# Kernel tuning notes

Hardware: AMD Instinct MI355X
Metric: run time of the kernel (lower is better)

## Reference

```python
import jax, jax.numpy as jnp
import numpy as np


def conv1d(x, w, b, pad):
    # x: [B, C, L], w: [O, C, K], torch nn.Conv1d semantics (cross-correlation + bias)
    y = jax.lax.conv_general_dilated(
        x, w, window_strides=(1,), padding=[(pad, pad)],
        dimension_numbers=("NCH", "OIH", "NCH"))
    return y + b[None, :, None]


def setup_inputs() -> dict:
    key = jax.random.key(0)
    ks = jax.random.split(key, 11)
    B, C, L = 32, 4, 65536
    def rn(k, shape, fan_in):
        # kaiming-ish scale so activations stay sane
        return jax.random.normal(k, shape, dtype=jnp.float32) / np.sqrt(fan_in)
    return {
        "x": jax.random.normal(ks[0], (B, C, L), dtype=jnp.float32),
        "w_motif": rn(ks[1], (40, 4, 51), 4 * 51),
        "b_motif": jnp.zeros((40,), jnp.float32),
        "w_reduce": rn(ks[2], (4, 40, 1), 40),
        "b_reduce": jnp.zeros((4,), jnp.float32),
        "w_fft": rn(ks[3], (4, 4, 401), 4 * 401),
        "b_fft": jnp.zeros((4,), jnp.float32),
        "w_expand": rn(ks[4], (40, 4, 1), 4),
        "b_expand": jnp.zeros((40,), jnp.float32),
        "w_effect": rn(ks[5], (2, 40, 601), 40 * 601),
        "b_effect": jnp.zeros((2,), jnp.float32),
    }


def reference(x, w_motif, b_motif, w_reduce, b_reduce, w_fft, b_fft,
              w_expand, b_expand, w_effect, b_effect):
    # motif layer + softplus
    y = jax.nn.softplus(conv1d(x, w_motif, b_motif, 25))          # [B,40,L]
    # synergy: factorized FFT-conv block (reduce 1x1 -> long conv -> expand 1x1)
    s = conv1d(y, w_reduce, b_reduce, 0)                          # [B,4,L]
    s = conv1d(s, w_fft, b_fft, 200)                              # [B,4,L]
    s = conv1d(s, w_expand, b_expand, 0)                          # [B,40,L]
    motifact = jax.nn.sigmoid(s) * y                              # gated
    # effect: long conv -> sigmoid
    y_pred = jax.nn.sigmoid(conv1d(motifact, w_effect, b_effect, 300))  # [B,2,L]
    return y_pred[:, :, 500:-500]
```

## Files before the change

### kernel.cpp

```cpp
#include <hip/hip_runtime.h>
#include <hip/hip_bf16.h>
#include <math.h>

#define LEN 65536
#define LOUT 64536
typedef __hip_bfloat16 bf16;
typedef __attribute__((ext_vector_type(8))) short short8;
typedef __attribute__((ext_vector_type(4))) float f32x4;

__device__ inline float b2f(bf16 h) { return __bfloat162float(h); }
__device__ inline bf16 f2b(float f) { return __float2bfloat16(f); }
__device__ inline float us2f(unsigned short u) { bf16 h = *(bf16*)&u; return __bfloat162float(h); }
__device__ inline float softplus_f(float v) {
    return fmaxf(v, 0.f) + __logf(1.f + __expf(-fabsf(v)));
}

__global__ __launch_bounds__(256) void k_x2b(const float* __restrict__ x,
                                             short* __restrict__ xb, int n8) {
    int i = blockIdx.x * 256 + threadIdx.x;
    if (i >= n8) return;
    const float* src = x + (size_t)i * 8;
    float4 f0 = *(const float4*)src;
    float4 f1 = *(const float4*)(src + 4);
    short8 v; bf16 h;
    h = f2b(f0.x); v[0] = *(short*)&h;
    h = f2b(f0.y); v[1] = *(short*)&h;
    h = f2b(f0.z); v[2] = *(short*)&h;
    h = f2b(f0.w); v[3] = *(short*)&h;
    h = f2b(f1.x); v[4] = *(short*)&h;
    h = f2b(f1.y); v[5] = *(short*)&h;
    h = f2b(f1.z); v[6] = *(short*)&h;
    h = f2b(f1.w); v[7] = *(short*)&h;
    *(short8*)(xb + (size_t)i * 8) = v;
}

__global__ __launch_bounds__(256) void k_prep_mot(const float* __restrict__ w_motif,
                                                  short* __restrict__ fragA) {
    int idx = blockIdx.x * 256 + threadIdx.x;
    if (idx >= 40 * 4 * 3 * 64 * 8) return;
    int i = idx & 7;
    int lane = (idx >> 3) & 63;
    int rest = idx >> 9;
    int qc = rest % 3; rest /= 3;
    int c = rest & 3; int o = rest >> 2;
    int dlt = lane & 15, kb = lane >> 4;
    int m = 32 * qc + 8 * kb + i;
    int k = m - 7 - dlt;
    float v = (k >= 0 && k < 51) ? w_motif[(o * 4 + c) * 51 + k] : 0.f;
    bf16 h = f2b(v);
    fragA[idx] = *(short*)&h;
}

#define MOT_BLKS 522
#define MOT_PAD  528
__global__ __launch_bounds__(256, 2) void k_motif_mfma(const short* __restrict__ xb,
        const short* __restrict__ fragA, const float* __restrict__ b_motif,
        const float* __restrict__ w_reduce, const float* __restrict__ b_reduce,
        bf16* __restrict__ y, bf16* __restrict__ s1, int b0) {
    __shared__ __align__(16) short bwin[4][MOT_PAD * 8];
    const int tid = threadIdx.x;
    const int lane = tid & 63, wv = tid >> 6;
    const int wg = blockIdx.x, bl = blockIdx.y;
    const int bg = b0 + bl;
    const int L0 = wg * 4096;
    const int win0 = L0 - 32;
    const int ln15 = lane & 15, lkb = lane >> 4;

    #pragma unroll 1
    for (int c = 0; c < 4; ++c) {
        const short* src = xb + ((size_t)bg * 4 + c) * LEN;
        for (int Lb = tid; Lb < MOT_BLKS; Lb += 256) {
            int gi = win0 + Lb * 8;
            short8 v;
            if (gi >= 0 && gi + 8 <= LEN) {
                v = *(const short8*)(src + gi);
            } else {
                #pragma unroll
                for (int j = 0; j < 8; ++j)
                    v[j] = (gi + j >= 0 && gi + j < LEN) ? src[gi + j] : (short)0;
            }
            int Pb = Lb ^ ((Lb >> 3) & 7);
            *(short8*)(&bwin[c][Pb * 8]) = v;
        }
    }
    __syncthreads();

    float s1a[4][4][4];
    #pragma unroll
    for (int nt = 0; nt < 4; ++nt)
        #pragma unroll
        for (int c = 0; c < 4; ++c) {
            float bc = b_reduce[c];
            #pragma unroll
            for (int j = 0; j < 4; ++j) s1a[nt][c][j] = bc;
        }

    #pragma unroll 1
    for (int og = 0; og < 10; ++og) {
        f32x4 acc[4][4];
        #pragma unroll
        for (int Mt = 0; Mt < 4; ++Mt)
            #pragma unroll
            for (int nt = 0; nt < 4; ++nt)
                acc[Mt][nt] = (f32x4){0.f, 0.f, 0.f, 0.f};

        #pragma unroll 1
        for (int c = 0; c < 4; ++c) {
            short8 afc[4][3];
            #pragma unroll
            for (int Mt = 0; Mt < 4; ++Mt)
                #pragma unroll
                for (int qc = 0; qc < 3; ++qc)
                    afc[Mt][qc] = *(const short8*)(fragA +
                        (size_t)(((og * 4 + Mt) * 12 + c * 3 + qc) * 64 + lane) * 8);
            #pragma unroll
            for (int nt = 0; nt < 4; ++nt) {
                const int tt = wv * 4 + nt;
                #pragma unroll
                for (int qc = 0; qc < 3; ++qc) {
                    int L = 32 * tt + 2 * ln15 + 4 * qc + lkb;
                    int P = L ^ ((L >> 3) & 7);
                    short8 bfr = *(const short8*)(&bwin[c][P * 8]);
                    #pragma unroll
                    for (int Mt = 0; Mt < 4; ++Mt)
                        acc[Mt][nt] = __builtin_amdgcn_mfma_f32_16x16x32_bf16(
                            afc[Mt][qc], bfr, acc[Mt][nt], 0, 0, 0);
                }
            }
        }

        #pragma unroll
        for (int Mt = 0; Mt < 4; ++Mt) {
            const int o = og * 4 + Mt;
            const float bb = b_motif[o];
            const float wr0 = w_reduce[0 * 40 + o], wr1 = w_reduce[1 * 40 + o];
            const float wr2 = w_reduce[2 * 40 + o], wr3 = w_reduce[3 * 40 + o];
            #pragma unroll
            for (int nt = 0; nt < 4; ++nt) {
                int tt = wv * 4 + nt;
                int pos = L0 + tt * 256 + 16 * ln15 + 4 * lkb;
                float v0 = softplus_f(acc[Mt][nt][0] + bb);
                float v1 = softplus_f(acc[Mt][nt][1] + bb);
                float v2 = softplus_f(acc[Mt][nt][2] + bb);
                float v3 = softplus_f(acc[Mt][nt][3] + bb);
                ushort4 st; bf16 h;
                h = f2b(v0); st.x = *(unsigned short*)&h;
                h = f2b(v1); st.y = *(unsigned short*)&h;
                h = f2b(v2); st.z = *(unsigned short*)&h;
                h = f2b(v3); st.w = *(unsigned short*)&h;
                *(ushort4*)(&y[((size_t)bl * 40 + o) * LEN + pos]) = st;
                s1a[nt][0][0] += wr0 * v0; s1a[nt][0][1] += wr0 * v1;
                s1a[nt][0][2] += wr0 * v2; s1a[nt][0][3] += wr0 * v3;
                s1a[nt][1][0] += wr1 * v0; s1a[nt][1][1] += wr1 * v1;
                s1a[nt][1][2] += wr1 * v2; s1a[nt][1][3] += wr1 * v3;
                s1a[nt][2][0] += wr2 * v0; s1a[nt][2][1] += wr2 * v1;
                s1a[nt][2][2] += wr2 * v2; s1a[nt][2][3] += wr2 * v3;
                s1a[nt][3][0] += wr3 * v0; s1a[nt][3][1] += wr3 * v1;
                s1a[nt][3][2] += wr3 * v2; s1a[nt][3][3] += wr3 * v3;
            }
        }
    }

    #pragma unroll
    for (int nt = 0; nt < 4; ++nt) {
        int tt = wv * 4 + nt;
        int pos = L0 + tt * 256 + 16 * ln15 + 4 * lkb;
        #pragma unroll
        for (int c = 0; c < 4; ++c) {
            ushort4 st; bf16 h;
            h = f2b(s1a[nt][c][0]); st.x = *(unsigned short*)&h;
            h = f2b(s1a[nt][c][1]); st.y = *(unsigned short*)&h;
            h = f2b(s1a[nt][c][2]); st.z = *(unsigned short*)&h;
            h = f2b(s1a[nt][c][3]); st.w = *(unsigned short*)&h;
            *(ushort4*)(&s1[((size_t)bl * 4 + c) * LEN + pos]) = st;
        }
    }
}

__global__ __launch_bounds__(256) void k_prep_fft(const float* __restrict__ w_fft,
                                                  short* __restrict__ fragA) {
    int idx = blockIdx.x * 256 + threadIdx.x;
    if (idx >= 4 * 7 * 4 * 2 * 64 * 8) return;
    int i = idx & 7;
    int lane = (idx >> 3) & 63;
    int rest = idx >> 9;
    int ql = rest & 1; rest >>= 1;
    int Mt = rest & 3; rest >>= 2;
    int qb = rest % 7; int c = rest / 7;
    int dlt = lane & 15, kb = lane >> 4;
    int kkp = 32 * (qb * 2 + ql) + 8 * kb + i;
    int kk = kkp - dlt;
    float v = (kk >= 0 && kk < 401) ? w_fft[(Mt * 4 + c) * 401 + kk] : 0.f;
    bf16 h = f2b(v);
    fragA[idx] = *(short*)&h;
}

#define FFT_BLKS 568
__global__ __launch_bounds__(256) void k_fft(const short* __restrict__ s1,
        const short* __restrict__ fragA, const float* __restrict__ b_fft,
        bf16* __restrict__ s2) {
    __shared__ __align__(16) short bwin[4][FFT_BLKS * 8];
    const int tid = threadIdx.x;
    const int lane = tid & 63, wv = tid >> 6;
    const int wg = blockIdx.x, bl = blockIdx.y;
    const int P0 = wg * 4096;
    const int win0 = P0 - 200;
    const int ln15 = lane & 15, lkb = lane >> 4;

    f32x4 acc[4][4];
    #pragma unroll
    for (int Mt = 0; Mt < 4; ++Mt)
        #pragma unroll
        for (int nt = 0; nt < 4; ++nt)
            acc[Mt][nt] = (f32x4){0.f, 0.f, 0.f, 0.f};

    #pragma unroll 1
    for (int cl = 0; cl < 4; ++cl) {
        const short* src = s1 + ((size_t)bl * 4 + cl) * LEN;
        for (int Lb = tid; Lb < FFT_BLKS; Lb += 256) {
            int gi = win0 + Lb * 8;
            short8 v;
            if (gi >= 0 && gi + 8 <= LEN) {
                v = *(const short8*)(src + gi);
            } else {
                #pragma unroll
                for (int j = 0; j < 8; ++j)
                    v[j] = (gi + j >= 0 && gi + j < LEN) ? src[gi + j] : (short)0;
            }
            int Pb = Lb ^ ((Lb >> 3) & 7);
            *(short8*)(&bwin[cl][Pb * 8]) = v;
        }
    }
    __syncthreads();

    #pragma unroll 1
    for (int cl = 0; cl < 4; ++cl) {
        #pragma unroll 1
        for (int qb = 0; qb < 7; ++qb) {
            short8 af[4][2];
            #pragma unroll
            for (int Mt = 0; Mt < 4; ++Mt)
                #pragma unroll
                for (int ql = 0; ql < 2; ++ql)
                    af[Mt][ql] = *(const short8*)(fragA +
                        (size_t)((((cl * 7 + qb) * 4 + Mt) * 2 + ql) * 64 + lane) * 8);
            #pragma unroll
            for (int nt = 0; nt < 4; ++nt) {
                const int tt = wv * 4 + nt;
                #pragma unroll
                for (int ql = 0; ql < 2; ++ql) {
                    int qc = qb * 2 + ql;
                    int L = 2 * ln15 + lkb + 4 * qc + 32 * tt;
                    int P = L ^ ((L >> 3) & 7);
                    short8 bfr = *(const short8*)(&bwin[cl][P * 8]);
                    #pragma unroll
                    for (int Mt = 0; Mt < 4; ++Mt)
                        acc[Mt][nt] = __builtin_amdgcn_mfma_f32_16x16x32_bf16(
                            af[Mt][ql], bfr, acc[Mt][nt], 0, 0, 0);
                }
            }
        }
    }

    #pragma unroll
    for (int Mt = 0; Mt < 4; ++Mt) {
        float bb = b_fft[Mt];
        #pragma unroll
        for (int nt = 0; nt < 4; ++nt) {
            int tt = wv * 4 + nt;
            int pos = P0 + tt * 256 + 16 * ln15 + 4 * lkb;
            ushort4 st; bf16 h;
            h = f2b(acc[Mt][nt][0] + bb); st.x = *(unsigned short*)&h;
            h = f2b(acc[Mt][nt][1] + bb); st.y = *(unsigned short*)&h;
            h = f2b(acc[Mt][nt][2] + bb); st.z = *(unsigned short*)&h;
            h = f2b(acc[Mt][nt][3] + bb); st.w = *(unsigned short*)&h;
            *(ushort4*)(&s2[((size_t)bl * 4 + Mt) * LEN + pos]) = st;
        }
    }
}

__global__ __launch_bounds__(256) void k_prep(const float* __restrict__ w_eff,
                                              short* __restrict__ fragA) {
    int idx = blockIdx.x * 256 + threadIdx.x;
    if (idx >= 40 * 4 * 2 * 5 * 64 * 8) return;
    int i = idx & 7;
    int lane = (idx >> 3) & 63;
    int rest = idx >> 9;
    int ql = rest % 5; rest /= 5;
    int Mt = rest & 1; rest >>= 1;
    int qb = rest & 3; int c = rest >> 2;
    int q = qb * 5 + ql;
    int dlt = lane & 15, kb = lane >> 4;
    int kp = 32 * q + 8 * kb + i;
    int kk = kp - dlt;
    float v = (kk >= 0 && kk < 601) ? w_eff[(Mt * 40 + c) * 601 + kk] : 0.f;
    bf16 h = __float2bfloat16(v);
    fragA[idx] = *(short*)&h;
}

#define EFF_NBLK 336
#define EFF_SH (EFF_NBLK * 8)
__device__ __forceinline__ void eff_prefetch(const short* __restrict__ mact,
        size_t chanBase, int cc, int tid, int win0, short8 (&yreg)[2][4]) {
    #pragma unroll
    for (int it = 0; it < 2; ++it) {
        int Lb = tid + it * 256;
        if (Lb < EFF_NBLK) {
            int gi = win0 + Lb * 8;
            bool full = (gi + 8 <= LEN);
            #pragma unroll
            for (int ch = 0; ch < 4; ++ch) {
                const short* src = mact + (chanBase + cc * 4 + ch) * (size_t)LEN;
                short8 v = {0, 0, 0, 0, 0, 0, 0, 0};
                if (full) {
                    v = *(const short8*)(src + gi);
                } else {
                    #pragma unroll
                    for (int j = 0; j < 8; ++j)
                        v[j] = (gi + j < LEN) ? src[gi + j] : (short)0;
                }
                yreg[it][ch] = v;
            }
        }
    }
}

__global__ __launch_bounds__(256, 3) void k_effect(const short* __restrict__ mact,
        const short* __restrict__ s2,
        const short* __restrict__ fragA,
        const float* __restrict__ w_expand, const float* __restrict__ b_expand,
        float* __restrict__ part) {
    __shared__ __align__(16) char smem[2 * EFF_SH * 4 * 2 + 160 * 4 + 40 * 4];
    short (*bwin)[EFF_SH]  = (short(*)[EFF_SH])smem;
    short (*s2win)[EFF_SH] = (short(*)[EFF_SH])(smem + EFF_SH * 4 * 2);
    float* wexp = (float*)(smem + 2 * EFF_SH * 4 * 2);
    float* bexp = wexp + 160;
    float* red  = (float*)smem;

    const int tid = threadIdx.x;
    const int lane = tid & 63, wv = tid >> 6;
    const int wgl = blockIdx.x, bl = blockIdx.y, half = blockIdx.z;
    const int coff = half * 20;
    const int L0 = wgl * 2048;
    const int win0 = L0 + 200;
    const int ln15 = lane & 15, lkb = lane >> 4;
    const size_t chanBase = (size_t)bl * 40 + coff;

    if (tid < 160) wexp[tid] = w_expand[tid];
    if (tid < 40) bexp[tid] = b_expand[tid];
    #pragma unroll 1
    for (int c = 0; c < 4; ++c) {
        const short* sp = s2 + ((size_t)bl * 4 + c) * LEN;
        for (int Lb = tid; Lb < EFF_NBLK; Lb += 256) {
            int gi = win0 + Lb * 8;
            short8 v = {0, 0, 0, 0, 0, 0, 0, 0};
            if (gi + 8 <= LEN) {
                v = *(const short8*)(sp + gi);
            } else {
                #pragma unroll
                for (int j = 0; j < 8; ++j)
                    v[j] = (gi + j < LEN) ? sp[gi + j] : (short)0;
            }
            *(short8*)(&s2win[c][Lb * 8]) = v;
        }
    }

    f32x4 acc[2][8];
    #pragma unroll
    for (int Mt = 0; Mt < 2; ++Mt)
        #pragma unroll
        for (int tt = 0; tt < 8; ++tt)
            acc[Mt][tt] = (f32x4){0.f, 0.f, 0.f, 0.f};

    short8 yreg[2][4];
    eff_prefetch(mact, chanBase, 0, tid, win0, yreg);

    #pragma unroll 1
    for (int cc = 0; cc < 5; ++cc) {
        __syncthreads();
        #pragma unroll
        for (int it = 0; it < 2; ++it) {
            int Lb = tid + it * 256;
            if (Lb < EFF_NBLK) {
                float s2v[4][8];
                #pragma unroll
                for (int c = 0; c < 4; ++c) {
                    short8 sv = *(const short8*)(&s2win[c][Lb * 8]);
                    #pragma unroll
                    for (int j = 0; j < 8; ++j) s2v[c][j] = us2f((unsigned short)sv[j]);
                }
                int P = Lb ^ ((Lb >> 3) & 7);
                #pragma unroll
                for (int ch = 0; ch < 4; ++ch) {
                    int o = coff + cc * 4 + ch;
                    float w0 = wexp[o * 4 + 0], w1 = wexp[o * 4 + 1];
                    float w2 = wexp[o * 4 + 2], w3 = wexp[o * 4 + 3];
                    float be = bexp[o];
                    short8 w;
                    #pragma unroll
                    for (int j = 0; j < 8; ++j) {
                        float sg = be + w0 * s2v[0][j] + w1 * s2v[1][j]
                                      + w2 * s2v[2][j] + w3 * s2v[3][j];
                        float g = __builtin_amdgcn_rcpf(1.f + __expf(-sg));
                        float yv = us2f((unsigned short)yreg[it][ch][j]) * g;
                        bf16 h = f2b(yv);
                        w[j] = *(short*)&h;
                    }
                    *(short8*)(&bwin[ch][P * 8]) = w;
                }
            }
        }
        __syncthreads();
        if (cc < 4) eff_prefetch(mact, chanBase, cc + 1, tid, win0, yreg);
        const int cg = coff + cc * 4 + wv;
        #pragma unroll 1
        for (int qb = 0; qb < 4; ++qb) {
            short8 af[2][5];
            #pragma unroll
            for (int Mt = 0; Mt < 2; ++Mt)
                #pragma unroll
                for (int ql = 0; ql < 5; ++ql)
                    af[Mt][ql] = *(const short8*)(fragA +
                        (size_t)(((((cg * 4 + qb) * 2 + Mt) * 5 + ql) * 64 + lane) * 8));
            #pragma unroll
            for (int tt = 0; tt < 8; ++tt) {
                #pragma unroll
                for (int ql = 0; ql < 5; ++ql) {
                    int q = qb * 5 + ql;
                    int L = 32 * tt + 2 * ln15 + 4 * q + lkb;
                    int P = L ^ ((L >> 3) & 7);
                    short8 bfr = *(const short8*)(&bwin[wv][P * 8]);
                    acc[0][tt] = __builtin_amdgcn_mfma_f32_16x16x32_bf16(
                        af[0][ql], bfr, acc[0][tt], 0, 0, 0);
                    acc[1][tt] = __builtin_amdgcn_mfma_f32_16x16x32_bf16(
                        af[1][ql], bfr, acc[1][tt], 0, 0, 0);
                }
            }
        }
    }

    __syncthreads();
    if (wv == 1 || wv == 3) {
        float* p = red + (wv >> 1) * 4096;
        #pragma unroll
        for (int Mt = 0; Mt < 2; ++Mt)
            #pragma unroll
            for (int tt = 0; tt < 8; ++tt)
                *(f32x4*)(p + (Mt * 8 + tt) * 256 + lane * 4) = acc[Mt][tt];
    }
    __syncthreads();
    if (wv == 0 || wv == 2) {
        float* p = red + (wv >> 1) * 4096;
        #pragma unroll
        for (int Mt = 0; Mt < 2; ++Mt)
            #pragma unroll
            for (int tt = 0; tt < 8; ++tt)
                acc[Mt][tt] += *(const f32x4*)(p + (Mt * 8 + tt) * 256 + lane * 4);
    }
    __syncthreads();
    if (wv == 2) {
        #pragma unroll
        for (int Mt = 0; Mt < 2; ++Mt)
            #pragma unroll
            for (int tt = 0; tt < 8; ++tt)
                *(f32x4*)(red + (Mt * 8 + tt) * 256 + lane * 4) = acc[Mt][tt];
    }
    __syncthreads();
    if (wv == 0) {
        #pragma unroll
        for (int Mt = 0; Mt < 2; ++Mt) {
            #pragma unroll
            for (int tt = 0; tt < 8; ++tt) {
                f32x4 a = acc[Mt][tt];
                a += *(const f32x4*)(red + (Mt * 8 + tt) * 256 + lane * 4);
                int pos = L0 + tt * 256 + 16 * ln15 + 4 * lkb;
                float4 st; st.x = a[0]; st.y = a[1]; st.z = a[2]; st.w = a[3];
                *(float4*)(&part[(((size_t)bl * 2 + half) * 2 + Mt) * LEN + pos]) = st;
            }
        }
    }
}

__global__ __launch_bounds__(256) void k_comb(const float* __restrict__ part,
        const float* __restrict__ b_eff, float* __restrict__ out, int b0) {
    const int tid = threadIdx.x;
    const int bl = blockIdx.y, bg = b0 + bl;
    int l4 = (blockIdx.x * 256 + tid) * 4;
    if (l4 >= LOUT) return;
    #pragma unroll
    for (int Mt = 0; Mt < 2; ++Mt) {
        float bb = b_eff[Mt];
        float4 p0 = *(const float4*)(&part[(((size_t)bl * 2 + 0) * 2 + Mt) * LEN + l4]);
        float4 p1 = *(const float4*)(&part[(((size_t)bl * 2 + 1) * 2 + Mt) * LEN + l4]);
        float4 st;
        st.x = __builtin_amdgcn_rcpf(1.f + __expf(-(p0.x + p1.x + bb)));
        st.y = __builtin_amdgcn_rcpf(1.f + __expf(-(p0.y + p1.y + bb)));
        st.z = __builtin_amdgcn_rcpf(1.f + __expf(-(p0.z + p1.z + bb)));
        st.w = __builtin_amdgcn_rcpf(1.f + __expf(-(p0.w + p1.w + bb)));
        *(float4*)(&out[((size_t)bg * 2 + Mt) * LOUT + l4]) = st;
    }
}

extern "C" void kernel_launch(void* const* d_in, const int* in_sizes, int n_in,
                              void* d_out, int out_size, void* d_ws, size_t ws_size,
                              hipStream_t stream) {
    const float* x        = (const float*)d_in[0];
    const float* w_motif  = (const float*)d_in[1];
    const float* b_motif  = (const float*)d_in[2];
    const float* w_reduce = (const float*)d_in[3];
    const float* b_reduce = (const float*)d_in[4];
    const float* w_fft    = (const float*)d_in[5];
    const float* b_fft    = (const float*)d_in[6];
    const float* w_expand = (const float*)d_in[7];
    const float* b_expand = (const float*)d_in[8];
    const float* w_eff    = (const float*)d_in[9];
    const float* b_eff    = (const float*)d_in[10];
    float* out = (float*)d_out;

    const size_t FRAGA_EFF = (size_t)40 * 4 * 2 * 5 * 64 * 8 * 2;
    const size_t FRAGA_FFT = (size_t)4 * 7 * 4 * 2 * 64 * 8 * 2;
    const size_t FRAGA_MOT = (size_t)40 * 4 * 3 * 64 * 8 * 2;
    const size_t XB_B      = (size_t)32 * 4 * LEN * 2;
    const size_t HEAD = FRAGA_EFF + FRAGA_FFT + FRAGA_MOT + XB_B;

    short* fragA_eff = (short*)d_ws;
    short* fragA_fft = (short*)((char*)d_ws + FRAGA_EFF);
    short* fragA_mot = (short*)((char*)d_ws + FRAGA_EFF + FRAGA_FFT);
    short* xb        = (short*)((char*)d_ws + FRAGA_EFF + FRAGA_FFT + FRAGA_MOT);
    char*  rest      = (char*)d_ws + HEAD;

    const size_t PB_Y = (size_t)40 * LEN * 2;
    const size_t PB_S = (size_t)4 * LEN * 2;
    const size_t PERB = PB_Y + 2 * PB_S + (size_t)2 * 2 * LEN * 4;
    size_t avail = (ws_size > HEAD) ? (ws_size - HEAD) : 0;
    int nb = (int)(avail / PERB);
    if (nb > 32) nb = 32;
    if (nb < 1) nb = 1;

    bf16*  y    = (bf16*)rest;
    bf16*  s1   = (bf16*)(rest + PB_Y * (size_t)nb);
    bf16*  s2   = (bf16*)(rest + (PB_Y + PB_S) * (size_t)nb);
    float* part = (float*)(rest + (PB_Y + 2 * PB_S) * (size_t)nb);

    hipLaunchKernelGGL(k_prep,     dim3(3200), dim3(256), 0, stream, w_eff, fragA_eff);
    hipLaunchKernelGGL(k_prep_fft, dim3(448),  dim3(256), 0, stream, w_fft, fragA_fft);
    hipLaunchKernelGGL(k_prep_mot, dim3(960),  dim3(256), 0, stream, w_motif, fragA_mot);
    hipLaunchKernelGGL(k_x2b,      dim3(4096), dim3(256), 0, stream, x, xb,
                       (int)(32 * 4 * LEN / 8));

    for (int b0 = 0; b0 < 32; b0 += nb) {
        int nbb = (32 - b0 < nb) ? (32 - b0) : nb;
        hipLaunchKernelGGL(k_motif_mfma, dim3(16, nbb), dim3(256), 0, stream,
                           xb, fragA_mot, b_motif, w_reduce, b_reduce, y, s1, b0);
        hipLaunchKernelGGL(k_fft, dim3(16, nbb), dim3(256), 0, stream,
                           (const short*)s1, fragA_fft, b_fft, s2);
        hipLaunchKernelGGL(k_effect, dim3(32, nbb, 2), dim3(256), 0, stream,
                           (const short*)y, (const short*)s2, fragA_eff,
                           w_expand, b_expand, part);
        hipLaunchKernelGGL(k_comb, dim3(64, nbb), dim3(256), 0, stream,
                           part, b_eff, out, b0);
    }
}
```

Baseline: 393.2 us.

## Remap effect-conv MFMA tiling to 4 M-tiles by 4 N-tiles with 32 delta rows

Changes the Toeplitz MFMA decomposition of the 601-tap effect convolution. Each A tile now covers 32 output shifts (two 16-row M-tiles per output channel) over 20 K-steps, where before it covered 16 shifts over 20 q-steps across 8 N-tiles. Each B fragment loaded from LDS now feeds 4 MFMAs instead of 2, which halves LDS B reads per MFMA and changes how the weight fragments are packed. The cost is a weight fragment table twice as large, read from global/L2 each K-step, and a Toeplitz expansion with more zero padding.

Result: no change. 395.0 us (+0.4%).

```diff
diff --git a/kernel.cpp b/kernel.cpp
--- a/kernel.cpp
+++ b/kernel.cpp
@@ -282,18 +282,18 @@
 __global__ __launch_bounds__(256) void k_prep(const float* __restrict__ w_eff,
                                               short* __restrict__ fragA) {
     int idx = blockIdx.x * 256 + threadIdx.x;
-    if (idx >= 40 * 4 * 2 * 5 * 64 * 8) return;
+    if (idx >= 40 * 20 * 4 * 64 * 8) return;
     int i = idx & 7;
     int lane = (idx >> 3) & 63;
     int rest = idx >> 9;
-    int ql = rest % 5; rest /= 5;
-    int Mt = rest & 1; rest >>= 1;
-    int qb = rest & 3; int c = rest >> 2;
-    int q = qb * 5 + ql;
-    int dlt = lane & 15, kb = lane >> 4;
-    int kp = 32 * q + 8 * kb + i;
+    int Mt = rest & 3; rest >>= 2;
+    int ks = rest % 20; int c = rest / 20;
+    int row16 = lane & 15, kb = lane >> 4;
+    int dlt = 16 * (Mt & 1) + row16;
+    int o = Mt >> 1;
+    int kp = 32 * ks + 8 * kb + i;
     int kk = kp - dlt;
-    float v = (kk >= 0 && kk < 601) ? w_eff[(Mt * 40 + c) * 601 + kk] : 0.f;
+    float v = (kk >= 0 && kk < 601) ? w_eff[(o * 40 + c) * 601 + kk] : 0.f;
     bf16 h = __float2bfloat16(v);
     fragA[idx] = *(short*)&h;
 }
@@ -365,12 +365,12 @@
         }
     }
 
-    f32x4 acc[2][8];
-    #pragma unroll
-    for (int Mt = 0; Mt < 2; ++Mt)
-        #pragma unroll
-        for (int tt = 0; tt < 8; ++tt)
-            acc[Mt][tt] = (f32x4){0.f, 0.f, 0.f, 0.f};
+    f32x4 acc[4][4];
+    #pragma unroll
+    for (int Mt = 0; Mt < 4; ++Mt)
+        #pragma unroll
+        for (int nt = 0; nt < 4; ++nt)
+            acc[Mt][nt] = (f32x4){0.f, 0.f, 0.f, 0.f};
 
     short8 yreg[2][4];
     eff_prefetch(mact, chanBase, 0, tid, win0, yreg);
@@ -414,27 +414,21 @@
         if (cc < 4) eff_prefetch(mact, chanBase, cc + 1, tid, win0, yreg);
         const int cg = coff + cc * 4 + wv;
         #pragma unroll 1
-        for (int qb = 0; qb < 4; ++qb) {
-            short8 af[2][5];
-            #pragma unroll
-            for (int Mt = 0; Mt < 2; ++Mt)
-                #pragma unroll
-                for (int ql = 0; ql < 5; ++ql)
-                    af[Mt][ql] = *(const short8*)(fragA +
-                        (size_t)(((((cg * 4 + qb) * 2 + Mt) * 5 + ql) * 64 + lane) * 8));
-            #pragma unroll
-            for (int tt = 0; tt < 8; ++tt) {
-                #pragma unroll
-                for (int ql = 0; ql < 5; ++ql) {
-                    int q = qb * 5 + ql;
-                    int L = 32 * tt + 2 * ln15 + 4 * q + lkb;
-                    int P = L ^ ((L >> 3) & 7);
-                    short8 bfr = *(const short8*)(&bwin[wv][P * 8]);
-                    acc[0][tt] = __builtin_amdgcn_mfma_f32_16x16x32_bf16(
-                        af[0][ql], bfr, acc[0][tt], 0, 0, 0);
-                    acc[1][tt] = __builtin_amdgcn_mfma_f32_16x16x32_bf16(
-                        af[1][ql], bfr, acc[1][tt], 0, 0, 0);
-                }
+        for (int ks = 0; ks < 20; ++ks) {
+            short8 af[4];
+            #pragma unroll
+            for (int Mt = 0; Mt < 4; ++Mt)
+                af[Mt] = *(const short8*)(fragA +
+                    (size_t)(((cg * 20 + ks) * 4 + Mt) * 64 + lane) * 8);
+            #pragma unroll
+            for (int nt = 0; nt < 4; ++nt) {
+                int L = 64 * nt + 4 * ln15 + 4 * ks + lkb;
+                int P = L ^ ((L >> 3) & 7);
+                short8 bfr = *(const short8*)(&bwin[wv][P * 8]);
+                #pragma unroll
+                for (int Mt = 0; Mt < 4; ++Mt)
+                    acc[Mt][nt] = __builtin_amdgcn_mfma_f32_16x16x32_bf16(
+                        af[Mt], bfr, acc[Mt][nt], 0, 0, 0);
             }
         }
     }
@@ -443,39 +437,40 @@
     if (wv == 1 || wv == 3) {
         float* p = red + (wv >> 1) * 4096;
         #pragma unroll
-        for (int Mt = 0; Mt < 2; ++Mt)
-            #pragma unroll
-            for (int tt = 0; tt < 8; ++tt)
-                *(f32x4*)(p + (Mt * 8 + tt) * 256 + lane * 4) = acc[Mt][tt];
+        for (int Mt = 0; Mt < 4; ++Mt)
+            #pragma unroll
+            for (int nt = 0; nt < 4; ++nt)
+                *(f32x4*)(p + (Mt * 4 + nt) * 256 + lane * 4) = acc[Mt][nt];
     }
     __syncthreads();
     if (wv == 0 || wv == 2) {
         float* p = red + (wv >> 1) * 4096;
         #pragma unroll
-        for (int Mt = 0; Mt < 2; ++Mt)
-            #pragma unroll
-            for (int tt = 0; tt < 8; ++tt)
-                acc[Mt][tt] += *(const f32x4*)(p + (Mt * 8 + tt) * 256 + lane * 4);
+        for (int Mt = 0; Mt < 4; ++Mt)
+            #pragma unroll
+            for (int nt = 0; nt < 4; ++nt)
+                acc[Mt][nt] += *(const f32x4*)(p + (Mt * 4 + nt) * 256 + lane * 4);
     }
     __syncthreads();
     if (wv == 2) {
         #pragma unroll
-        for (int Mt = 0; Mt < 2; ++Mt)
-            #pragma unroll
-            for (int tt = 0; tt < 8; ++tt)
-                *(f32x4*)(red + (Mt * 8 + tt) * 256 + lane * 4) = acc[Mt][tt];
+        for (int Mt = 0; Mt < 4; ++Mt)
+            #pragma unroll
+            for (int nt = 0; nt < 4; ++nt)
+                *(f32x4*)(red + (Mt * 4 + nt) * 256 + lane * 4) = acc[Mt][nt];
     }
     __syncthreads();
     if (wv == 0) {
         #pragma unroll
-        for (int Mt = 0; Mt < 2; ++Mt) {
-            #pragma unroll
-            for (int tt = 0; tt < 8; ++tt) {
-                f32x4 a = acc[Mt][tt];
-                a += *(const f32x4*)(red + (Mt * 8 + tt) * 256 + lane * 4);
-                int pos = L0 + tt * 256 + 16 * ln15 + 4 * lkb;
+        for (int Mt = 0; Mt < 4; ++Mt) {
+            const int o = Mt >> 1;
+            #pragma unroll
+            for (int nt = 0; nt < 4; ++nt) {
+                f32x4 a = acc[Mt][nt];
+                a += *(const f32x4*)(red + (Mt * 4 + nt) * 256 + lane * 4);
+                int pos = L0 + 512 * nt + 32 * ln15 + 16 * (Mt & 1) + 4 * lkb;
                 float4 st; st.x = a[0]; st.y = a[1]; st.z = a[2]; st.w = a[3];
-                *(float4*)(&part[(((size_t)bl * 2 + half) * 2 + Mt) * LEN + pos]) = st;
+                *(float4*)(&part[(((size_t)bl * 2 + half) * 2 + o) * LEN + pos]) = st;
             }
         }
     }
@@ -517,7 +512,7 @@
     const float* b_eff    = (const float*)d_in[10];
     float* out = (float*)d_out;
 
-    const size_t FRAGA_EFF = (size_t)40 * 4 * 2 * 5 * 64 * 8 * 2;
+    const size_t FRAGA_EFF = (size_t)40 * 20 * 4 * 64 * 8 * 2;
     const size_t FRAGA_FFT = (size_t)4 * 7 * 4 * 2 * 64 * 8 * 2;
     const size_t FRAGA_MOT = (size_t)40 * 4 * 3 * 64 * 8 * 2;
     const size_t XB_B      = (size_t)32 * 4 * LEN * 2;
@@ -542,7 +537,7 @@
     bf16*  s2   = (bf16*)(rest + (PB_Y + PB_S) * (size_t)nb);
     float* part = (float*)(rest + (PB_Y + 2 * PB_S) * (size_t)nb);
 
-    hipLaunchKernelGGL(k_prep,     dim3(3200), dim3(256), 0, stream, w_eff, fragA_eff);
+    hipLaunchKernelGGL(k_prep,     dim3(6400), dim3(256), 0, stream, w_eff, fragA_eff);
     hipLaunchKernelGGL(k_prep_fft, dim3(448),  dim3(256), 0, stream, w_fft, fragA_fft);
     hipLaunchKernelGGL(k_prep_mot, dim3(960),  dim3(256), 0, stream, w_motif, fragA_mot);
     hipLaunchKernelGGL(k_x2b,      dim3(4096), dim3(256), 0, stream, x, xb,
```

## Make each wave build its own gated channel window and drop block barriers

Applied to the files above, without the earlier changes.

Each of the four waves now computes the sigmoid-gated motif activation only for the channel it later consumes in the MFMA loop. It prefetches that channel's data itself with a per-lane strided layout. Because every wave writes and reads only its own bwin slice, the two __syncthreads per channel-chunk iteration are removed and a single barrier after the shared s2 window load remains. The intent is to cut block-wide synchronisation stalls and let waves drift independently. The cost is that s2win is re-read by each wave, and the per-lane work split (6 iterations over 336 blocks) is somewhat uneven.

New measurement: 402.4 us. 2.3% more time.

```diff
diff --git a/kernel.cpp b/kernel.cpp
--- a/kernel.cpp
+++ b/kernel.cpp
@@ -300,28 +300,23 @@
 
 #define EFF_NBLK 336
 #define EFF_SH (EFF_NBLK * 8)
-__device__ __forceinline__ void eff_prefetch(const short* __restrict__ mact,
-        size_t chanBase, int cc, int tid, int win0, short8 (&yreg)[2][4]) {
-    #pragma unroll
-    for (int it = 0; it < 2; ++it) {
-        int Lb = tid + it * 256;
+__device__ __forceinline__ void eff_prefetch_w(const short* __restrict__ src,
+        int lane, int win0, short8 (&yreg)[6]) {
+    #pragma unroll
+    for (int it = 0; it < 6; ++it) {
+        int Lb = it * 64 + lane;
+        short8 v = {0, 0, 0, 0, 0, 0, 0, 0};
         if (Lb < EFF_NBLK) {
             int gi = win0 + Lb * 8;
-            bool full = (gi + 8 <= LEN);
-            #pragma unroll
-            for (int ch = 0; ch < 4; ++ch) {
-                const short* src = mact + (chanBase + cc * 4 + ch) * (size_t)LEN;
-                short8 v = {0, 0, 0, 0, 0, 0, 0, 0};
-                if (full) {
-                    v = *(const short8*)(src + gi);
-                } else {
-                    #pragma unroll
-                    for (int j = 0; j < 8; ++j)
-                        v[j] = (gi + j < LEN) ? src[gi + j] : (short)0;
-                }
-                yreg[it][ch] = v;
-            }
-        }
+            if (gi + 8 <= LEN) {
+                v = *(const short8*)(src + gi);
+            } else {
+                #pragma unroll
+                for (int j = 0; j < 8; ++j)
+                    v[j] = (gi + j < LEN) ? src[gi + j] : (short)0;
+            }
+        }
+        yreg[it] = v;
     }
 }
 
@@ -372,46 +367,46 @@
         for (int tt = 0; tt < 8; ++tt)
             acc[Mt][tt] = (f32x4){0.f, 0.f, 0.f, 0.f};
 
-    short8 yreg[2][4];
-    eff_prefetch(mact, chanBase, 0, tid, win0, yreg);
+    short8 yreg[6];
+    eff_prefetch_w(mact + (chanBase + 0 * 4 + wv) * (size_t)LEN, lane, win0, yreg);
+    __syncthreads();
 
     #pragma unroll 1
     for (int cc = 0; cc < 5; ++cc) {
-        __syncthreads();
-        #pragma unroll
-        for (int it = 0; it < 2; ++it) {
-            int Lb = tid + it * 256;
-            if (Lb < EFF_NBLK) {
-                float s2v[4][8];
-                #pragma unroll
-                for (int c = 0; c < 4; ++c) {
-                    short8 sv = *(const short8*)(&s2win[c][Lb * 8]);
+        {
+            const int o = coff + cc * 4 + wv;
+            const float w0 = wexp[o * 4 + 0], w1 = wexp[o * 4 + 1];
+            const float w2 = wexp[o * 4 + 2], w3 = wexp[o * 4 + 3];
+            const float be = bexp[o];
+            #pragma unroll
+            for (int it = 0; it < 6; ++it) {
+                int Lb = it * 64 + lane;
+                if (Lb < EFF_NBLK) {
+                    float s2v[4][8];
                     #pragma unroll
-                    for (int j = 0; j < 8; ++j) s2v[c][j] = us2f((unsigned short)sv[j]);
-                }
-                int P = Lb ^ ((Lb >> 3) & 7);
-                #pragma unroll
-                for (int ch = 0; ch < 4; ++ch) {
-                    int o = coff + cc * 4 + ch;
-                    float w0 = wexp[o * 4 + 0], w1 = wexp[o * 4 + 1];
-                    float w2 = wexp[o * 4 + 2], w3 = wexp[o * 4 + 3];
-                    float be = bexp[o];
+                    for (int c = 0; c < 4; ++c) {
+                        short8 sv = *(const short8*)(&s2win[c][Lb * 8]);
+                        #pragma unroll
+                        for (int j = 0; j < 8; ++j) s2v[c][j] = us2f((unsigned short)sv[j]);
+                    }
                     short8 w;
                     #pragma unroll
                     for (int j = 0; j < 8; ++j) {
                         float sg = be + w0 * s2v[0][j] + w1 * s2v[1][j]
                                       + w2 * s2v[2][j] + w3 * s2v[3][j];
                         float g = __builtin_amdgcn_rcpf(1.f + __expf(-sg));
-                        float yv = us2f((unsigned short)yreg[it][ch][j]) * g;
+                        float yv = us2f((unsigned short)yreg[it][j]) * g;
                         bf16 h = f2b(yv);
                         w[j] = *(short*)&h;
                     }
-                    *(short8*)(&bwin[ch][P * 8]) = w;
+                    int P = Lb ^ ((Lb >> 3) & 7);
+                    *(short8*)(&bwin[wv][P * 8]) = w;
                 }
             }
         }
-        __syncthreads();
-        if (cc < 4) eff_prefetch(mact, chanBase, cc + 1, tid, win0, yreg);
+        if (cc < 4)
+            eff_prefetch_w(mact + (chanBase + (cc + 1) * 4 + wv) * (size_t)LEN,
+                           lane, win0, yreg);
         const int cg = coff + cc * 4 + wv;
         #pragma unroll 1
         for (int qb = 0; qb < 4; ++qb) {
```

## Split effect conv channels into five groups and store bf16 partials

Applied to the files above, without the earlier changes.

The effect convolution grid now splits its 40 input channels into five groups of 8 instead of two groups of 20, raising the block count from 64 to 160 per batch chunk and shortening each block's loop. Partial sums are stored as bf16 rather than fp32, and the combine kernel sums five bf16 partials before the sigmoid. This is meant to improve occupancy and reduce tail effects in the dominant kernel. In exchange each block repeats the s2 window load and setup more often, the combine kernel reads more partial arrays, and bf16 partials lose precision.

Measured after the change: 425.0 us. 1.08x slower.

```diff
diff --git a/kernel.cpp b/kernel.cpp
--- a/kernel.cpp
+++ b/kernel.cpp
@@ -329,7 +329,7 @@
         const short* __restrict__ s2,
         const short* __restrict__ fragA,
         const float* __restrict__ w_expand, const float* __restrict__ b_expand,
-        float* __restrict__ part) {
+        bf16* __restrict__ part) {
     __shared__ __align__(16) char smem[2 * EFF_SH * 4 * 2 + 160 * 4 + 40 * 4];
     short (*bwin)[EFF_SH]  = (short(*)[EFF_SH])smem;
     short (*s2win)[EFF_SH] = (short(*)[EFF_SH])(smem + EFF_SH * 4 * 2);
@@ -339,8 +339,8 @@
 
     const int tid = threadIdx.x;
     const int lane = tid & 63, wv = tid >> 6;
-    const int wgl = blockIdx.x, bl = blockIdx.y, half = blockIdx.z;
-    const int coff = half * 20;
+    const int wgl = blockIdx.x, bl = blockIdx.y, part5 = blockIdx.z;
+    const int coff = part5 * 8;
     const int L0 = wgl * 2048;
     const int win0 = L0 + 200;
     const int ln15 = lane & 15, lkb = lane >> 4;
@@ -376,7 +376,7 @@
     eff_prefetch(mact, chanBase, 0, tid, win0, yreg);
 
     #pragma unroll 1
-    for (int cc = 0; cc < 5; ++cc) {
+    for (int cc = 0; cc < 2; ++cc) {
         __syncthreads();
         #pragma unroll
         for (int it = 0; it < 2; ++it) {
@@ -411,7 +411,7 @@
             }
         }
         __syncthreads();
-        if (cc < 4) eff_prefetch(mact, chanBase, cc + 1, tid, win0, yreg);
+        if (cc < 1) eff_prefetch(mact, chanBase, cc + 1, tid, win0, yreg);
         const int cg = coff + cc * 4 + wv;
         #pragma unroll 1
         for (int qb = 0; qb < 4; ++qb) {
@@ -474,14 +474,18 @@
                 f32x4 a = acc[Mt][tt];
                 a += *(const f32x4*)(red + (Mt * 8 + tt) * 256 + lane * 4);
                 int pos = L0 + tt * 256 + 16 * ln15 + 4 * lkb;
-                float4 st; st.x = a[0]; st.y = a[1]; st.z = a[2]; st.w = a[3];
-                *(float4*)(&part[(((size_t)bl * 2 + half) * 2 + Mt) * LEN + pos]) = st;
-            }
-        }
-    }
-}
-
-__global__ __launch_bounds__(256) void k_comb(const float* __restrict__ part,
+                ushort4 st; bf16 h;
+                h = f2b(a[0]); st.x = *(unsigned short*)&h;
+                h = f2b(a[1]); st.y = *(unsigned short*)&h;
+                h = f2b(a[2]); st.z = *(unsigned short*)&h;
+                h = f2b(a[3]); st.w = *(unsigned short*)&h;
+                *(ushort4*)(&part[(((size_t)bl * 5 + part5) * 2 + Mt) * LEN + pos]) = st;
+            }
+        }
+    }
+}
+
+__global__ __launch_bounds__(256) void k_comb(const bf16* __restrict__ part,
         const float* __restrict__ b_eff, float* __restrict__ out, int b0) {
     const int tid = threadIdx.x;
     const int bl = blockIdx.y, bg = b0 + bl;
@@ -490,13 +494,18 @@
     #pragma unroll
     for (int Mt = 0; Mt < 2; ++Mt) {
         float bb = b_eff[Mt];
-        float4 p0 = *(const float4*)(&part[(((size_t)bl * 2 + 0) * 2 + Mt) * LEN + l4]);
-        float4 p1 = *(const float4*)(&part[(((size_t)bl * 2 + 1) * 2 + Mt) * LEN + l4]);
+        float a0 = bb, a1 = bb, a2 = bb, a3 = bb;
+        #pragma unroll
+        for (int h5 = 0; h5 < 5; ++h5) {
+            ushort4 v = *(const ushort4*)((const unsigned short*)part +
+                (((size_t)bl * 5 + h5) * 2 + Mt) * LEN + l4);
+            a0 += us2f(v.x); a1 += us2f(v.y); a2 += us2f(v.z); a3 += us2f(v.w);
+        }
         float4 st;
-        st.x = __builtin_amdgcn_rcpf(1.f + __expf(-(p0.x + p1.x + bb)));
-        st.y = __builtin_amdgcn_rcpf(1.f + __expf(-(p0.y + p1.y + bb)));
-        st.z = __builtin_amdgcn_rcpf(1.f + __expf(-(p0.z + p1.z + bb)));
-        st.w = __builtin_amdgcn_rcpf(1.f + __expf(-(p0.w + p1.w + bb)));
+        st.x = __builtin_amdgcn_rcpf(1.f + __expf(-a0));
+        st.y = __builtin_amdgcn_rcpf(1.f + __expf(-a1));
+        st.z = __builtin_amdgcn_rcpf(1.f + __expf(-a2));
+        st.w = __builtin_amdgcn_rcpf(1.f + __expf(-a3));
         *(float4*)(&out[((size_t)bg * 2 + Mt) * LOUT + l4]) = st;
     }
 }
@@ -531,7 +540,8 @@
 
     const size_t PB_Y = (size_t)40 * LEN * 2;
     const size_t PB_S = (size_t)4 * LEN * 2;
-    const size_t PERB = PB_Y + 2 * PB_S + (size_t)2 * 2 * LEN * 4;
+    const size_t PB_P = (size_t)5 * 2 * LEN * 2;
+    const size_t PERB = PB_Y + 2 * PB_S + PB_P;
     size_t avail = (ws_size > HEAD) ? (ws_size - HEAD) : 0;
     int nb = (int)(avail / PERB);
     if (nb > 32) nb = 32;
@@ -540,7 +550,7 @@
     bf16*  y    = (bf16*)rest;
     bf16*  s1   = (bf16*)(rest + PB_Y * (size_t)nb);
     bf16*  s2   = (bf16*)(rest + (PB_Y + PB_S) * (size_t)nb);
-    float* part = (float*)(rest + (PB_Y + 2 * PB_S) * (size_t)nb);
+    bf16*  part = (bf16*)(rest + (PB_Y + 2 * PB_S) * (size_t)nb);
 
     hipLaunchKernelGGL(k_prep,     dim3(3200), dim3(256), 0, stream, w_eff, fragA_eff);
     hipLaunchKernelGGL(k_prep_fft, dim3(448),  dim3(256), 0, stream, w_fft, fragA_fft);
@@ -554,7 +564,7 @@
                            xb, fragA_mot, b_motif, w_reduce, b_reduce, y, s1, b0);
         hipLaunchKernelGGL(k_fft, dim3(16, nbb), dim3(256), 0, stream,
                            (const short*)s1, fragA_fft, b_fft, s2);
-        hipLaunchKernelGGL(k_effect, dim3(32, nbb, 2), dim3(256), 0, stream,
+        hipLaunchKernelGGL(k_effect, dim3(32, nbb, 5), dim3(256), 0, stream,
                            (const short*)y, (const short*)s2, fragA_eff,
                            w_expand, b_expand, part);
         hipLaunchKernelGGL(k_comb, dim3(64, nbb), dim3(256), 0, stream,
```
